# Kernel tuning notes

Hardware: AMD Instinct MI355X
Metric: run time of the kernel (lower is better)

The kernel has to match this reference:

```python
import jax, jax.numpy as jnp
import numpy as np
from jax import lax

B, D, H, W, C = 2, 144, 64, 160, 32
P = 300000
EPS = 1e-4   # scn BatchNormLeakyReLU default eps
LEAK = 0.2


def setup_inputs() -> dict:
    key = jax.random.key(0)
    ks = jax.random.split(key, 10)
    features = jax.random.normal(ks[0], (P, C), jnp.float32)
    b = jax.random.randint(ks[1], (P, 1), 0, B)
    x = jax.random.randint(ks[2], (P, 1), 0, D)
    y = jax.random.randint(ks[3], (P, 1), 0, H)
    z = jax.random.randint(ks[4], (P, 1), 0, W)
    coords = jnp.concatenate([b, x, y, z], axis=1).astype(jnp.int32)

    def conv_w(k, cin, cout):
        return jax.random.normal(k, (2, 2, 2, cin, cout), jnp.float32) / np.float32(np.sqrt(8 * cin))

    return {
        "features": features, "coords": coords,
        "w1": conv_w(ks[5], C, 64),  "g1": jnp.ones((64,), jnp.float32),  "b1": jnp.zeros((64,), jnp.float32),
        "w2": conv_w(ks[6], 64, 96), "g2": jnp.ones((96,), jnp.float32),  "b2": jnp.zeros((96,), jnp.float32),
        "w3": conv_w(ks[7], 96, 128),"g3": jnp.ones((128,), jnp.float32), "b3": jnp.zeros((128,), jnp.float32),
        "w4": conv_w(ks[8], 128, 1),
    }


def _densify(features, coords):
    # scn.InputLayer mode=4: average features of duplicate coordinates.
    lin = ((coords[:, 0] * D + coords[:, 1]) * H + coords[:, 2]) * W + coords[:, 3]
    grid = jnp.zeros((B * D * H * W, C), features.dtype).at[lin].add(features)
    cnt = jnp.zeros((B * D * H * W,), features.dtype).at[lin].add(1.0)
    grid = grid / jnp.maximum(cnt, 1.0)[:, None]
    x = grid.reshape(B, D, H, W, C)
    mask = (cnt > 0).astype(features.dtype).reshape(B, D, H, W, 1)
    return x, mask


def _conv2s2(x, w):
    # scn.Convolution(dim=3, filter=2, stride=2, bias=False): inactive inputs are zero,
    # so dense VALID conv reproduces values at active output sites exactly.
    return lax.conv_general_dilated(x, w, (2, 2, 2), 'VALID',
                                    dimension_numbers=('NDHWC', 'DHWIO', 'NDHWC'))


def _downsample_mask(mask):
    # Output site is active iff any input in its 2x2x2 window is active.
    return lax.reduce_window(mask, 0.0, lax.max, (1, 2, 2, 2, 1), (1, 2, 2, 2, 1), 'VALID')


def _block(x, mask, w, gamma, beta):
    x = _conv2s2(x, w)
    mask = _downsample_mask(mask)
    n = jnp.maximum(jnp.sum(mask), 1.0)
    # x is exactly zero at inactive sites, so sums over all sites == sums over active sites.
    mean = jnp.sum(x, axis=(0, 1, 2, 3)) / n
    var = jnp.sum(x * x, axis=(0, 1, 2, 3)) / n - mean * mean
    y = (x - mean) * (gamma * lax.rsqrt(var + EPS)) + beta
    y = jnp.where(y > 0, y, LEAK * y) * mask   # LeakyReLU on active sites, zero elsewhere
    return y, mask


def reference(features, coords, w1, g1, b1, w2, g2, b2, w3, g3, b3, w4):
    x, mask = _densify(features, coords)
    x, mask = _block(x, mask, w1, g1, b1)
    x, mask = _block(x, mask, w2, g2, b2)
    x, mask = _block(x, mask, w3, g3, b3)
    x = _conv2s2(x, w4)                 # [B, 9, 4, 10, 1]
    mask = _downsample_mask(mask)
    return jax.nn.sigmoid(x) * mask     # sigmoid of features; inactive sites zeroed
```

## Files before the change

kernel.cpp:

```cpp
#include <hip/hip_runtime.h>
#include <math.h>

#define PNUM 300000
#define B_ 2
#define D0 144
#define H0 64
#define W0 160
#define NVOX (B_*D0*H0*W0)

#define D1 72
#define H1 32
#define W1 80
#define N1S (B_*D1*H1*W1)

#define D2 36
#define H2 16
#define W2 40
#define N2S (B_*D2*H2*W2)

#define D3 18
#define H3 8
#define W3 20
#define N3S (B_*D3*H3*W3)

#define D4 9
#define H4 4
#define W4 10
#define N4S (B_*D4*H4*W4)

#define EPS_ 1e-4f
#define LEAK_ 0.2f

typedef __attribute__((ext_vector_type(8))) short v8s;
typedef __attribute__((ext_vector_type(4))) float v4f;

typedef unsigned short ushort_t;
typedef unsigned int uint_t;
typedef unsigned long long ull_t;

__device__ __forceinline__ ushort_t f2b(float f) {
  union { float f; uint_t u; } x; x.f = f;
  uint_t r = x.u + 0x7FFFu + ((x.u >> 16) & 1u);
  return (ushort_t)(r >> 16);
}
__device__ __forceinline__ float b2f(ushort_t h) {
  union { uint_t u; float f; } x; x.u = ((uint_t)h) << 16; return x.f;
}
__device__ __forceinline__ uint_t bn2(uint_t w, float s0, float h0, float s1, float h1,
                                      float msk) {
  float v0 = b2f((ushort_t)(w & 0xffff));
  float v1 = b2f((ushort_t)(w >> 16));
  v0 = fmaf(v0, s0, h0); v1 = fmaf(v1, s1, h1);
  v0 = fmaxf(v0, LEAK_ * v0) * msk;
  v1 = fmaxf(v1, LEAK_ * v1) * msk;
  return (uint_t)f2b(v0) | ((uint_t)f2b(v1) << 16);
}

template <int DD, int HH, int WW>
__device__ __forceinline__ int okey(int p) {
  int b = p / (DD*HH*WW); int r = p - b*(DD*HH*WW);
  int x = r / (HH*WW); r -= x*(HH*WW);
  int y = r / WW; int z = r - y*WW;
  return (((((b*(DD/2) + (x >> 1))*(HH/2) + (y >> 1))*(WW/2)) + (z >> 1)) << 3)
         | ((x & 1) << 2) | ((y & 1) << 1) | (z & 1);
}

#define OFF_CNT     0
#define OFF_STATS   2949120
#define OFF_CURSOR  2965504
#define OFF_DKLIST  5914624
#define OFF_WT1     6514624
#define OFF_WT2     6522816
#define OFF_WT3     6555584
#define OFF_AFEATB  6621120
#define OFF_X1B     11421120
#define OFF_X2B     23217600
#define OFF_X3B     26166720
#define OFF_M1      26535360
#define OFF_M2      26904000
#define OFF_M3      26950080

#define ST_S1P  0
#define ST_Q1P  2560
#define ST_S2P  5120
#define ST_Q2P  7424
#define ST_S3P  9728
#define ST_Q3P  12032
#define ST_N2P  14336
#define ST_N3P  14368
#define ST_GCUR 14400
#define ST_PK   14404

__device__ __forceinline__ int voxkey(int b, int x, int y, int z) {
  int p = ((b*D1 + (x >> 1))*H1 + (y >> 1))*W1 + (z >> 1);
  int oct = ((x & 1) << 2) | ((y & 1) << 1) | (z & 1);
  return p*8 + oct;
}

#define NB_COUNT 1172
#define NB_PREPW 832
#define NB_STZ   16
__global__ __launch_bounds__(256) void k_front(
    const int* __restrict__ coords, int* __restrict__ cnt,
    const float* __restrict__ w1, const float* __restrict__ w2,
    const float* __restrict__ w3,
    ushort_t* __restrict__ wt1, ushort_t* __restrict__ wt2,
    ushort_t* __restrict__ wt3, float* __restrict__ stz) {
  int bb = blockIdx.x, t = threadIdx.x;
  if (bb < NB_COUNT) {
    int i = bb * 256 + t;
    if (i < PNUM) {
      int4 c = *(const int4*)(coords + i*4);
      atomicAdd(&cnt[voxkey(c.x, c.y, c.z, c.w)], 1);
    }
  } else if (bb < NB_COUNT + NB_PREPW) {
    int idx = (bb - NB_COUNT) * 256 + t;
    if (idx < 16384) {
      int c = idx >> 11, r = idx & 2047;
      int co = r >> 5, kk = r & 31;
      wt1[idx] = f2b(w1[(c*32 + kk)*64 + co]);
    } else if (idx < 16384 + 65536) {
      int i = idx - 16384;
      int c = i >> 12, r = i & 4095;
      int co = r >> 5, kk = r & 31;
      int k = c*32 + kk;
      wt2[i] = (co < 96) ? f2b(w2[k*96 + co]) : 0;
    } else {
      int i = idx - 81920;
      int c = i >> 12, r = i & 4095;
      int co = r >> 5, kk = r & 31;
      int k = c*32 + kk;
      int ch = k >> 7, ci = k & 127;
      wt3[i] = (ci < 96) ? f2b(w3[(ch*96 + ci)*128 + co]) : 0;
    }
  } else {
    int off = ((bb - NB_COUNT - NB_PREPW) * 256 + t) * 4;
    *(float4*)(stz + off) = make_float4(0.f, 0.f, 0.f, 0.f);
  }
}

__global__ __launch_bounds__(1024) void k_alloc(const int* __restrict__ cnt,
                                                int* __restrict__ cursor,
                                                float* __restrict__ m1b,
                                                int* __restrict__ dklist,
                                                int* __restrict__ gcur,
                                                ull_t* __restrict__ pkctr) {
  __shared__ ull_t wsum[16];
  __shared__ int slotBase;
  __shared__ ull_t pkBase;
  int t = threadIdx.x;
  int idx0 = blockIdx.x * 16384 + t * 16;
  int c[16];
  int tsum = 0, dup = 0;
#pragma unroll
  for (int j = 0; j < 4; j++) {
    int4 cv = *(const int4*)(cnt + idx0 + j*4);
    c[j*4+0] = cv.x; c[j*4+1] = cv.y; c[j*4+2] = cv.z; c[j*4+3] = cv.w;
    tsum += cv.x + cv.y + cv.z + cv.w;
  }
#pragma unroll
  for (int j = 0; j < 16; j++) dup += (c[j] > 1) ? 1 : 0;
  uint_t m0 = 0, m1m = 0;
#pragma unroll
  for (int j = 0; j < 8; j++) { if (c[j] > 0) m0 |= (1u << j); }
#pragma unroll
  for (int j = 0; j < 8; j++) { if (c[8+j] > 0) m1m |= (1u << j); }
  int pa = ((m0 != 0) ? 1 : 0) + ((m1m != 0) ? 1 : 0);
  ull_t sv = ((ull_t)(uint_t)tsum << 32) | (ull_t)(uint_t)((pa << 16) | dup);
  int lane = t & 63, wid = t >> 6;
  ull_t incl = sv;
#pragma unroll
  for (int o = 1; o < 64; o <<= 1) {
    ull_t v = __shfl_up(incl, o);
    if (lane >= o) incl += v;
  }
  if (lane == 63) wsum[wid] = incl;
  __syncthreads();
  if (t == 0) {
    ull_t tot = 0;
#pragma unroll
    for (int w = 0; w < 16; w++) { ull_t v = wsum[w]; wsum[w] = tot; tot += v; }
    slotBase = atomicAdd(gcur, (int)(tot >> 32));
    uint_t pk = (uint_t)(tot & 0xffffffffULL);
    pkBase = atomicAdd(pkctr, ((ull_t)(pk >> 16) << 32) | (ull_t)(pk & 0xffff));
  }
  __syncthreads();
  ull_t excl = wsum[wid] + incl - sv;
  int st = slotBase + (int)(excl >> 32);
  uint_t pkl = (uint_t)(excl & 0xffffffffULL);
  int koff = (int)(pkBase & 0xffffffffULL) + (int)(pkl & 0xffff);
#pragma unroll
  for (int j = 0; j < 4; j++) {
    int4 sv2;
    sv2.x = st; st += c[j*4+0];
    sv2.y = st; st += c[j*4+1];
    sv2.z = st; st += c[j*4+2];
    sv2.w = st; st += c[j*4+3];
    *(int4*)(cursor + idx0 + j*4) = sv2;
  }
  int p0 = idx0 >> 3;
  m1b[okey<D1,H1,W1>(p0)]     = (m0 != 0) ? 1.f : 0.f;
  m1b[okey<D1,H1,W1>(p0 + 1)] = (m1m != 0) ? 1.f : 0.f;
#pragma unroll
  for (int j = 0; j < 16; j++)
    if (c[j] > 1) dklist[koff++] = idx0 + j;
}

__global__ __launch_bounds__(256) void k_scatter(const int* __restrict__ coords,
                                                 const float* __restrict__ feat,
                                                 const int* __restrict__ cnt,
                                                 int* __restrict__ cursor,
                                                 ushort_t* __restrict__ afb) {
  int i = blockIdx.x * 256 + threadIdx.x;
  if (i >= PNUM) return;
  int4 c = *(const int4*)(coords + i*4);
  int key = voxkey(c.x, c.y, c.z, c.w);
  int slot = atomicAdd(&cursor[key], 1);
  float inv = 1.f / (float)cnt[key];
  const float4* fp = (const float4*)(feat + (size_t)i * 32);
  uint_t o[16];
#pragma unroll
  for (int q = 0; q < 8; q++) {
    float4 v = fp[q];
    o[q*2]   = (uint_t)f2b(v.x*inv) | ((uint_t)f2b(v.y*inv) << 16);
    o[q*2+1] = (uint_t)f2b(v.z*inv) | ((uint_t)f2b(v.w*inv) << 16);
  }
  uint4* dst = (uint4*)(afb + (size_t)slot * 32);
  dst[0] = make_uint4(o[0], o[1], o[2], o[3]);
  dst[1] = make_uint4(o[4], o[5], o[6], o[7]);
  dst[2] = make_uint4(o[8], o[9], o[10], o[11]);
  dst[3] = make_uint4(o[12], o[13], o[14], o[15]);
}

__global__ __launch_bounds__(256) void k_davg(const int* __restrict__ cnt,
                                              const int* __restrict__ cursor,
                                              const int* __restrict__ dklist,
                                              const int* __restrict__ ndup,
                                              ushort_t* __restrict__ afb) {
  int gid = blockIdx.x * 256 + threadIdx.x;
  int j = gid >> 3;
  if (j >= ndup[0]) return;
  int key = dklist[j];
  int c = cnt[key];
  int s0 = cursor[key] - c;
  int q = (gid & 7) * 4;
  float a0 = 0.f, a1 = 0.f, a2 = 0.f, a3 = 0.f;
  for (int i = 0; i < c; i++) {
    uint2 u = *(const uint2*)(afb + (size_t)(s0 + i) * 32 + q);
    a0 += b2f((ushort_t)(u.x & 0xffff)); a1 += b2f((ushort_t)(u.x >> 16));
    a2 += b2f((ushort_t)(u.y & 0xffff)); a3 += b2f((ushort_t)(u.y >> 16));
  }
  uint2 o;
  o.x = (uint_t)f2b(a0) | ((uint_t)f2b(a1) << 16);
  o.y = (uint_t)f2b(a2) | ((uint_t)f2b(a3) << 16);
  *(uint2*)(afb + (size_t)s0 * 32 + q) = o;
}

__global__ __launch_bounds__(256) void k_conv1m(
    const ushort_t* __restrict__ afb, const int* __restrict__ cnt,
    const int* __restrict__ cursor, const ushort_t* __restrict__ wtg,
    ushort_t* __restrict__ x1b, float* __restrict__ sp, float* __restrict__ qp) {
  __shared__ __align__(16) ushort_t wlds[16384];
  __shared__ int cst[128*9];
  __shared__ int okl[128];
  __shared__ int pact[128];
  __shared__ float redS[4][64], redQ[4][64];
  int t = threadIdx.x;
#pragma unroll
  for (int i = 0; i < 8; i++)
    ((uint4*)wlds)[t + i*256] = ((const uint4*)wtg)[t + i*256];
  if (t < 128) {
    int p = blockIdx.x * 128 + t;
    okl[t] = okey<D1,H1,W1>(p);
    const int4* cp = (const int4*)(cnt + (size_t)p*8);
    const int4* up = (const int4*)(cursor + (size_t)p*8);
    int4 c0 = cp[0], c1 = cp[1], u0 = up[0], u1 = up[1];
    cst[t*9 + 0] = (c0.x > 0) ? (u0.x - c0.x) : -1;
    cst[t*9 + 1] = (c0.y > 0) ? (u0.y - c0.y) : -1;
    cst[t*9 + 2] = (c0.z > 0) ? (u0.z - c0.z) : -1;
    cst[t*9 + 3] = (c0.w > 0) ? (u0.w - c0.w) : -1;
    cst[t*9 + 4] = (c1.x > 0) ? (u1.x - c1.x) : -1;
    cst[t*9 + 5] = (c1.y > 0) ? (u1.y - c1.y) : -1;
    cst[t*9 + 6] = (c1.z > 0) ? (u1.z - c1.z) : -1;
    cst[t*9 + 7] = (c1.w > 0) ? (u1.w - c1.w) : -1;
    pact[t] = (c0.x + c0.y + c0.z + c0.w + c1.x + c1.y + c1.z + c1.w) > 0 ? 1 : 0;
  }
  __syncthreads();
  int lane = t & 63, wv = t >> 6;
  int l15 = lane & 15, q = lane >> 4;
  int SB = wv * 32;
  v8s a[8][2];
#pragma unroll
  for (int c = 0; c < 8; c++) {
#pragma unroll
    for (int mt = 0; mt < 2; mt++) {
      int site = SB + mt*16 + l15;
      int sp2 = cst[site*9 + c];
      v8s av = {0,0,0,0,0,0,0,0};
      if (sp2 >= 0) av = *(const v8s*)(afb + (size_t)sp2*32 + q*8);
      a[c][mt] = av;
    }
  }
  v4f acc[2][4];
#pragma unroll
  for (int i = 0; i < 2; i++)
#pragma unroll
    for (int j = 0; j < 4; j++) acc[i][j] = (v4f){0.f, 0.f, 0.f, 0.f};
#pragma unroll
  for (int c = 0; c < 8; c++) {
    v8s b[4];
#pragma unroll
    for (int nt = 0; nt < 4; nt++)
      b[nt] = *(const v8s*)&wlds[c*2048 + (nt*16 + l15)*32 + q*8];
#pragma unroll
    for (int mt = 0; mt < 2; mt++)
#pragma unroll
      for (int nt = 0; nt < 4; nt++)
        acc[mt][nt] = __builtin_amdgcn_mfma_f32_16x16x32_bf16(a[c][mt], b[nt], acc[mt][nt], 0, 0, 0);
  }
  float ss[4] = {0,0,0,0}, sq[4] = {0,0,0,0};
#pragma unroll
  for (int mt = 0; mt < 2; mt++) {
#pragma unroll
    for (int nt = 0; nt < 4; nt++) {
#pragma unroll
      for (int r = 0; r < 4; r++) {
        int sl = SB + mt*16 + q*4 + r;
        ushort_t h = f2b(acc[mt][nt][r]);
        float v = b2f(h);
        if (pact[sl]) x1b[(size_t)okl[sl]*64 + nt*16 + l15] = h;
        ss[nt] += v; sq[nt] += v*v;
      }
    }
  }
#pragma unroll
  for (int nt = 0; nt < 4; nt++) {
    float v1 = ss[nt], v2 = sq[nt];
    v1 += __shfl_xor(v1, 16); v1 += __shfl_xor(v1, 32);
    v2 += __shfl_xor(v2, 16); v2 += __shfl_xor(v2, 32);
    if (lane < 16) { redS[wv][nt*16 + l15] = v1; redQ[wv][nt*16 + l15] = v2; }
  }
  __syncthreads();
  if (t < 64) {
    float s = redS[0][t] + redS[1][t] + redS[2][t] + redS[3][t];
    float qq = redQ[0][t] + redQ[1][t] + redQ[2][t] + redQ[3][t];
    int row = (blockIdx.x & 31) * 80;
    atomicAdd(&sp[row + t], s);
    atomicAdd(&qp[row + t], qq);
  }
}

template <int CSTRIDE, int CIN_REAL, bool NINT, int NROW, int INSTR,
          int DO, int HO, int WO>
__global__ __launch_bounds__(256) void k_convm(
    const ushort_t* __restrict__ xin, const float* __restrict__ mprev,
    const ushort_t* __restrict__ wtg,
    const float* __restrict__ gam, const float* __restrict__ bet,
    const float* __restrict__ spin, const float* __restrict__ qpin,
    const void* __restrict__ ncnt, const float* __restrict__ npin,
    ushort_t* __restrict__ xout, float* __restrict__ osum, float* __restrict__ osq,
    float* __restrict__ mout, float* __restrict__ npart) {
  const int NCHUNK = CSTRIDE / 4;
  __shared__ __align__(16) float sc[CSTRIDE], sh[CSTRIDE];
  __shared__ float cmask[64*9];
  __shared__ int okl[64];
  __shared__ float redS[4][64], redQ[4][64];
  int t = threadIdx.x;
  if (t < CSTRIDE) {
    float scv = 0.f, shv = 0.f;
    if (t < CIN_REAL) {
      float n;
      if (NINT) n = fmaxf((float)((const int*)ncnt)[0], 1.0f);
      else {
        float nn = 0.f;
        for (int r = 0; r < 32; r++) nn += npin[r];
        n = fmaxf(nn, 1.0f);
      }
      float s1 = 0.f, q1 = 0.f;
      for (int r = 0; r < NROW; r++) { s1 += spin[r*INSTR + t]; q1 += qpin[r*INSTR + t]; }
      float mean = s1 / n;
      float var = q1 / n - mean * mean;
      float s = gam[t] * rsqrtf(var + EPS_);
      scv = s; shv = bet[t] - mean * s;
    }
    sc[t] = scv; sh[t] = shv;
  }
#pragma unroll
  for (int ii = 0; ii < 2; ii++) {
    int idx = t + ii*256;
    cmask[(idx >> 3)*9 + (idx & 7)] = mprev[(size_t)blockIdx.x * 512 + idx];
  }
  if (t < 64) okl[t] = okey<DO,HO,WO>(blockIdx.x * 64 + t);
  __syncthreads();
  int lane = t & 63, wv = t >> 6;
  int l15 = lane & 15, q = lane >> 4;
  int SB = (wv & 1) * 32, NB = (wv >> 1) * 64;
  size_t gbase = (size_t)blockIdx.x * 512;
  v4f acc[2][4];
#pragma unroll
  for (int i = 0; i < 2; i++)
#pragma unroll
    for (int j = 0; j < 4; j++) acc[i][j] = (v4f){0.f, 0.f, 0.f, 0.f};
  uint4 rawN[2]; float mskN[2]; v8s bN[4];
#pragma unroll
  for (int mt = 0; mt < 2; mt++) {
    int site = SB + mt*16 + l15;
    float m = cmask[site*9];
    uint4 rv = make_uint4(0, 0, 0, 0);
    if (m > 0.f) rv = *(const uint4*)(xin + (gbase + site*8) * CSTRIDE + q*8);
    rawN[mt] = rv; mskN[mt] = m;
  }
#pragma unroll
  for (int nt = 0; nt < 4; nt++)
    bN[nt] = *(const v8s*)(wtg + (NB + nt*16 + l15)*32 + q*8);
#pragma unroll
  for (int c = 0; c < NCHUNK; c++) {
    uint4 raw[2] = {rawN[0], rawN[1]};
    float mskc[2] = {mskN[0], mskN[1]};
    v8s b[4] = {bN[0], bN[1], bN[2], bN[3]};
    if (c + 1 < NCHUNK) {
      int ch1 = ((c+1) * 32) / CSTRIDE;
      int cio1 = ((c+1) * 32) % CSTRIDE + q * 8;
#pragma unroll
      for (int mt = 0; mt < 2; mt++) {
        int site = SB + mt*16 + l15;
        float m = cmask[site*9 + ch1];
        uint4 rv = make_uint4(0, 0, 0, 0);
        if (m > 0.f) rv = *(const uint4*)(xin + (gbase + site*8 + ch1) * CSTRIDE + cio1);
        rawN[mt] = rv; mskN[mt] = m;
      }
#pragma unroll
      for (int nt = 0; nt < 4; nt++)
        bN[nt] = *(const v8s*)(wtg + (size_t)(c+1)*4096 + (NB + nt*16 + l15)*32 + q*8);
    }
    int cio = (c * 32) % CSTRIDE + q * 8;
    float4 sc0 = *(const float4*)&sc[cio];
    float4 sc1 = *(const float4*)&sc[cio + 4];
    float4 sh0 = *(const float4*)&sh[cio];
    float4 sh1 = *(const float4*)&sh[cio + 4];
    v8s a[2];
#pragma unroll
    for (int mt = 0; mt < 2; mt++) {
      int4 pk;
      pk.x = (int)bn2(raw[mt].x, sc0.x, sh0.x, sc0.y, sh0.y, mskc[mt]);
      pk.y = (int)bn2(raw[mt].y, sc0.z, sh0.z, sc0.w, sh0.w, mskc[mt]);
      pk.z = (int)bn2(raw[mt].z, sc1.x, sh1.x, sc1.y, sh1.y, mskc[mt]);
      pk.w = (int)bn2(raw[mt].w, sc1.z, sh1.z, sc1.w, sh1.w, mskc[mt]);
      a[mt] = *(v8s*)&pk;
    }
#pragma unroll
    for (int mt = 0; mt < 2; mt++)
#pragma unroll
      for (int nt = 0; nt < 4; nt++)
        acc[mt][nt] = __builtin_amdgcn_mfma_f32_16x16x32_bf16(a[mt], b[nt], acc[mt][nt], 0, 0, 0);
  }
  float ss[4] = {0,0,0,0}, sq[4] = {0,0,0,0};
#pragma unroll
  for (int mt = 0; mt < 2; mt++) {
#pragma unroll
    for (int nt = 0; nt < 4; nt++) {
#pragma unroll
      for (int r = 0; r < 4; r++) {
        int sl = SB + mt*16 + q*4 + r;
        ushort_t h = f2b(acc[mt][nt][r]);
        float v = b2f(h);
        xout[(size_t)okl[sl]*128 + NB + nt*16 + l15] = h;
        ss[nt] += v; sq[nt] += v*v;
      }
    }
  }
  if (t < 64) {
    bool act = false;
#pragma unroll
    for (int ch = 0; ch < 8; ch++) act |= (cmask[t*9 + ch] > 0.f);
    mout[okl[t]] = act ? 1.f : 0.f;
    unsigned long long bal = __ballot(act);
    if (t == 0) atomicAdd(&npart[blockIdx.x & 31], (float)__popcll(bal));
  }
#pragma unroll
  for (int nt = 0; nt < 4; nt++) {
    float v1 = ss[nt], v2 = sq[nt];
    v1 += __shfl_xor(v1, 16); v1 += __shfl_xor(v1, 32);
    v2 += __shfl_xor(v2, 16); v2 += __shfl_xor(v2, 32);
    if (lane < 16) { redS[wv][nt*16 + l15] = v1; redQ[wv][nt*16 + l15] = v2; }
  }
  __syncthreads();
  if (t < 128) {
    float s, qq;
    if (t < 64) { s = redS[0][t] + redS[1][t]; qq = redQ[0][t] + redQ[1][t]; }
    else        { s = redS[2][t-64] + redS[3][t-64]; qq = redQ[2][t-64] + redQ[3][t-64]; }
    int row = (blockIdx.x & 15) * 144;
    atomicAdd(&osum[row + t], s);
    atomicAdd(&osq[row + t], qq);
  }
}

__global__ __launch_bounds__(256) void k_final(
    const ushort_t* __restrict__ x3b, const float* __restrict__ m3b,
    const float* __restrict__ w4, const float* __restrict__ gam,
    const float* __restrict__ bet, const float* __restrict__ spin,
    const float* __restrict__ qpin, const float* __restrict__ npin,
    float* __restrict__ out) {
  __shared__ float sc[128], sh[128];
  __shared__ float msk[8];
  __shared__ float red[256];
  int t = threadIdx.x;
  if (t < 128) {
    float nn = 0.f;
    for (int r = 0; r < 32; r++) nn += npin[r];
    float n = fmaxf(nn, 1.0f);
    float s1 = 0.f, q1 = 0.f;
    for (int r = 0; r < 16; r++) { s1 += spin[r*144 + t]; q1 += qpin[r*144 + t]; }
    float mean = s1 / n;
    float var = q1 / n - mean * mean;
    float s = gam[t] * rsqrtf(var + EPS_);
    sc[t] = s; sh[t] = bet[t] - mean * s;
  }
  int g = blockIdx.x;
  if (t < 8) msk[t] = m3b[g*8 + t];
  __syncthreads();
  float acc = 0.f;
#pragma unroll
  for (int ii = 0; ii < 4; ii++) {
    int k = t + ii*256;
    int ch = k >> 7, ci = k & 127;
    float v = b2f(x3b[(size_t)(g*8 + ch)*128 + ci]);
    v = v * sc[ci] + sh[ci];
    v = (v > 0.f ? v : LEAK_ * v) * msk[ch];
    acc += v * w4[k];
  }
  red[t] = acc;
  __syncthreads();
  if (t < 128) red[t] += red[t + 128];
  __syncthreads();
  if (t < 64) {
    float v = red[t] + red[t + 64];
#pragma unroll
    for (int off = 32; off > 0; off >>= 1) v += __shfl_down(v, off);
    if (t == 0) {
      float any = (msk[0] + msk[1] + msk[2] + msk[3] + msk[4] + msk[5] + msk[6] + msk[7]) > 0.f ? 1.f : 0.f;
      out[g] = any / (1.0f + expf(-v));
    }
  }
}

extern "C" void kernel_launch(void* const* d_in, const int* in_sizes, int n_in,
                              void* d_out, int out_size, void* d_ws, size_t ws_size,
                              hipStream_t stream) {
  (void)in_sizes; (void)n_in; (void)out_size; (void)ws_size;
  const float* feat = (const float*)d_in[0];
  const int*   crd  = (const int*)d_in[1];
  const float* w1 = (const float*)d_in[2];
  const float* g1 = (const float*)d_in[3];
  const float* b1 = (const float*)d_in[4];
  const float* w2 = (const float*)d_in[5];
  const float* g2 = (const float*)d_in[6];
  const float* b2 = (const float*)d_in[7];
  const float* w3 = (const float*)d_in[8];
  const float* g3 = (const float*)d_in[9];
  const float* b3 = (const float*)d_in[10];
  const float* w4 = (const float*)d_in[11];
  float* out = (float*)d_out;
  float* ws  = (float*)d_ws;

  int*      cnt    = (int*)(ws + OFF_CNT);
  float*    st     = ws + OFF_STATS;
  int*      cursor = (int*)(ws + OFF_CURSOR);
  int*      dklist = (int*)(ws + OFF_DKLIST);
  ushort_t* wt1g   = (ushort_t*)(ws + OFF_WT1);
  ushort_t* wt2g   = (ushort_t*)(ws + OFF_WT2);
  ushort_t* wt3g   = (ushort_t*)(ws + OFF_WT3);
  ushort_t* afb    = (ushort_t*)(ws + OFF_AFEATB);
  ushort_t* x1b    = (ushort_t*)(ws + OFF_X1B);
  ushort_t* x2b    = (ushort_t*)(ws + OFF_X2B);
  ushort_t* x3b    = (ushort_t*)(ws + OFF_X3B);
  float*    m1b    = ws + OFF_M1;
  float*    m2b    = ws + OFF_M2;
  float*    m3b    = ws + OFF_M3;
  ull_t*    pkctr  = (ull_t*)(st + ST_PK);
  int*      ndup   = (int*)(st + ST_PK);
  int*      nactp  = (int*)(st + ST_PK + 1);

  hipMemsetAsync(cnt, 0, (size_t)NVOX * sizeof(int), stream);

  k_front<<<NB_COUNT + NB_PREPW + NB_STZ, 256, 0, stream>>>(
      crd, cnt, w1, w2, w3, wt1g, wt2g, wt3g, st);
  k_alloc<<<NVOX / 16384, 1024, 0, stream>>>(cnt, cursor, m1b, dklist,
                                             (int*)(st + ST_GCUR), pkctr);
  k_scatter<<<(PNUM + 255) / 256, 256, 0, stream>>>(crd, feat, cnt, cursor, afb);
  k_davg<<<4688, 256, 0, stream>>>(cnt, cursor, dklist, ndup, afb);
  k_conv1m<<<N1S / 128, 256, 0, stream>>>(afb, cnt, cursor, wt1g, x1b,
                                          st + ST_S1P, st + ST_Q1P);
  k_convm<64, 64, true, 32, 80, D2,H2,W2><<<N2S / 64, 256, 0, stream>>>(
      x1b, m1b, wt2g, g1, b1, st + ST_S1P, st + ST_Q1P, (const void*)nactp, nullptr,
      x2b, st + ST_S2P, st + ST_Q2P, m2b, st + ST_N2P);
  k_convm<128, 96, false, 16, 144, D3,H3,W3><<<N3S / 64, 256, 0, stream>>>(
      x2b, m2b, wt3g, g2, b2, st + ST_S2P, st + ST_Q2P, nullptr, st + ST_N2P,
      x3b, st + ST_S3P, st + ST_Q3P, m3b, st + ST_N3P);
  k_final<<<N4S, 256, 0, stream>>>(x3b, m3b, w4, g3, b3,
                                   st + ST_S3P, st + ST_Q3P, st + ST_N3P, out);
}
```

Measured before the change: 244.2 us.

## Fuse duplicate-voxel averaging into conv1 gather and drop davg kernel

Removes the k_davg kernel and the duplicate-key list built in k_alloc. Duplicate-coordinate sums are now accumulated directly while conv1 gathers its input, using per-site counts kept in shared memory. The scan in k_alloc is simplified to 32-bit with a separate active-count reduction. conv1 also iterates blocks in output-key order so x1b stores are contiguous, and it reuses the weight LDS for the reduction scratch. The cost is divergent extra loads inside the conv1 gather for duplicate sites, plus an added barrier.

```diff
diff --git a/kernel.cpp b/kernel.cpp
--- a/kernel.cpp
+++ b/kernel.cpp
@@ -68,7 +68,6 @@
 #define OFF_CNT     0
 #define OFF_STATS   2949120
 #define OFF_CURSOR  2965504
-#define OFF_DKLIST  5914624
 #define OFF_WT1     6514624
 #define OFF_WT2     6522816
 #define OFF_WT3     6555584
@@ -142,53 +141,49 @@
 __global__ __launch_bounds__(1024) void k_alloc(const int* __restrict__ cnt,
                                                 int* __restrict__ cursor,
                                                 float* __restrict__ m1b,
-                                                int* __restrict__ dklist,
                                                 int* __restrict__ gcur,
-                                                ull_t* __restrict__ pkctr) {
-  __shared__ ull_t wsum[16];
-  __shared__ int slotBase;
-  __shared__ ull_t pkBase;
+                                                int* __restrict__ nactp) {
+  __shared__ int wsum[16];
+  __shared__ int wpa[16];
+  __shared__ int blockBase;
   int t = threadIdx.x;
   int idx0 = blockIdx.x * 16384 + t * 16;
   int c[16];
-  int tsum = 0, dup = 0;
+  int tsum = 0;
 #pragma unroll
   for (int j = 0; j < 4; j++) {
     int4 cv = *(const int4*)(cnt + idx0 + j*4);
     c[j*4+0] = cv.x; c[j*4+1] = cv.y; c[j*4+2] = cv.z; c[j*4+3] = cv.w;
     tsum += cv.x + cv.y + cv.z + cv.w;
   }
-#pragma unroll
-  for (int j = 0; j < 16; j++) dup += (c[j] > 1) ? 1 : 0;
   uint_t m0 = 0, m1m = 0;
 #pragma unroll
   for (int j = 0; j < 8; j++) { if (c[j] > 0) m0 |= (1u << j); }
 #pragma unroll
   for (int j = 0; j < 8; j++) { if (c[8+j] > 0) m1m |= (1u << j); }
   int pa = ((m0 != 0) ? 1 : 0) + ((m1m != 0) ? 1 : 0);
-  ull_t sv = ((ull_t)(uint_t)tsum << 32) | (ull_t)(uint_t)((pa << 16) | dup);
   int lane = t & 63, wid = t >> 6;
-  ull_t incl = sv;
+  int incl = tsum;
 #pragma unroll
   for (int o = 1; o < 64; o <<= 1) {
-    ull_t v = __shfl_up(incl, o);
+    int v = __shfl_up(incl, o);
     if (lane >= o) incl += v;
   }
+  int pw = pa;
+#pragma unroll
+  for (int o = 1; o < 64; o <<= 1) pw += __shfl_xor(pw, o);
   if (lane == 63) wsum[wid] = incl;
+  if (lane == 0) wpa[wid] = pw;
   __syncthreads();
   if (t == 0) {
-    ull_t tot = 0;
-#pragma unroll
-    for (int w = 0; w < 16; w++) { ull_t v = wsum[w]; wsum[w] = tot; tot += v; }
-    slotBase = atomicAdd(gcur, (int)(tot >> 32));
-    uint_t pk = (uint_t)(tot & 0xffffffffULL);
-    pkBase = atomicAdd(pkctr, ((ull_t)(pk >> 16) << 32) | (ull_t)(pk & 0xffff));
-  }
-  __syncthreads();
-  ull_t excl = wsum[wid] + incl - sv;
-  int st = slotBase + (int)(excl >> 32);
-  uint_t pkl = (uint_t)(excl & 0xffffffffULL);
-  int koff = (int)(pkBase & 0xffffffffULL) + (int)(pkl & 0xffff);
+    int tot = 0, ptot = 0;
+#pragma unroll
+    for (int w = 0; w < 16; w++) { int v = wsum[w]; wsum[w] = tot; tot += v; ptot += wpa[w]; }
+    blockBase = atomicAdd(gcur, tot);
+    atomicAdd(nactp, ptot);
+  }
+  __syncthreads();
+  int st = blockBase + wsum[wid] + incl - tsum;
 #pragma unroll
   for (int j = 0; j < 4; j++) {
     int4 sv2;
@@ -201,9 +196,6 @@
   int p0 = idx0 >> 3;
   m1b[okey<D1,H1,W1>(p0)]     = (m0 != 0) ? 1.f : 0.f;
   m1b[okey<D1,H1,W1>(p0 + 1)] = (m1m != 0) ? 1.f : 0.f;
-#pragma unroll
-  for (int j = 0; j < 16; j++)
-    if (c[j] > 1) dklist[koff++] = idx0 + j;
 }
 
 __global__ __launch_bounds__(256) void k_scatter(const int* __restrict__ coords,
@@ -232,57 +224,39 @@
   dst[3] = make_uint4(o[12], o[13], o[14], o[15]);
 }
 
-__global__ __launch_bounds__(256) void k_davg(const int* __restrict__ cnt,
-                                              const int* __restrict__ cursor,
-                                              const int* __restrict__ dklist,
-                                              const int* __restrict__ ndup,
-                                              ushort_t* __restrict__ afb) {
-  int gid = blockIdx.x * 256 + threadIdx.x;
-  int j = gid >> 3;
-  if (j >= ndup[0]) return;
-  int key = dklist[j];
-  int c = cnt[key];
-  int s0 = cursor[key] - c;
-  int q = (gid & 7) * 4;
-  float a0 = 0.f, a1 = 0.f, a2 = 0.f, a3 = 0.f;
-  for (int i = 0; i < c; i++) {
-    uint2 u = *(const uint2*)(afb + (size_t)(s0 + i) * 32 + q);
-    a0 += b2f((ushort_t)(u.x & 0xffff)); a1 += b2f((ushort_t)(u.x >> 16));
-    a2 += b2f((ushort_t)(u.y & 0xffff)); a3 += b2f((ushort_t)(u.y >> 16));
-  }
-  uint2 o;
-  o.x = (uint_t)f2b(a0) | ((uint_t)f2b(a1) << 16);
-  o.y = (uint_t)f2b(a2) | ((uint_t)f2b(a3) << 16);
-  *(uint2*)(afb + (size_t)s0 * 32 + q) = o;
-}
-
 __global__ __launch_bounds__(256) void k_conv1m(
     const ushort_t* __restrict__ afb, const int* __restrict__ cnt,
     const int* __restrict__ cursor, const ushort_t* __restrict__ wtg,
     ushort_t* __restrict__ x1b, float* __restrict__ sp, float* __restrict__ qp) {
   __shared__ __align__(16) ushort_t wlds[16384];
   __shared__ int cst[128*9];
-  __shared__ int okl[128];
+  __shared__ ushort_t ccn[128*9];
   __shared__ int pact[128];
-  __shared__ float redS[4][64], redQ[4][64];
   int t = threadIdx.x;
 #pragma unroll
   for (int i = 0; i < 8; i++)
     ((uint4*)wlds)[t + i*256] = ((const uint4*)wtg)[t + i*256];
   if (t < 128) {
-    int p = blockIdx.x * 128 + t;
-    okl[t] = okey<D1,H1,W1>(p);
+    int ok = blockIdx.x * 128 + t;
+    int oct = ok & 7, qp2 = ok >> 3;
+    int b = qp2 / (D2*H2*W2); int r = qp2 - b*(D2*H2*W2);
+    int x2 = r / (H2*W2); r -= x2*(H2*W2);
+    int y2 = r / W2; int z2 = r - y2*W2;
+    int x = 2*x2 + ((oct >> 2) & 1);
+    int y = 2*y2 + ((oct >> 1) & 1);
+    int z = 2*z2 + (oct & 1);
+    int p = ((b*D1 + x)*H1 + y)*W1 + z;
     const int4* cp = (const int4*)(cnt + (size_t)p*8);
     const int4* up = (const int4*)(cursor + (size_t)p*8);
     int4 c0 = cp[0], c1 = cp[1], u0 = up[0], u1 = up[1];
-    cst[t*9 + 0] = (c0.x > 0) ? (u0.x - c0.x) : -1;
-    cst[t*9 + 1] = (c0.y > 0) ? (u0.y - c0.y) : -1;
-    cst[t*9 + 2] = (c0.z > 0) ? (u0.z - c0.z) : -1;
-    cst[t*9 + 3] = (c0.w > 0) ? (u0.w - c0.w) : -1;
-    cst[t*9 + 4] = (c1.x > 0) ? (u1.x - c1.x) : -1;
-    cst[t*9 + 5] = (c1.y > 0) ? (u1.y - c1.y) : -1;
-    cst[t*9 + 6] = (c1.z > 0) ? (u1.z - c1.z) : -1;
-    cst[t*9 + 7] = (c1.w > 0) ? (u1.w - c1.w) : -1;
+    cst[t*9 + 0] = (c0.x > 0) ? (u0.x - c0.x) : -1; ccn[t*9 + 0] = (ushort_t)c0.x;
+    cst[t*9 + 1] = (c0.y > 0) ? (u0.y - c0.y) : -1; ccn[t*9 + 1] = (ushort_t)c0.y;
+    cst[t*9 + 2] = (c0.z > 0) ? (u0.z - c0.z) : -1; ccn[t*9 + 2] = (ushort_t)c0.z;
+    cst[t*9 + 3] = (c0.w > 0) ? (u0.w - c0.w) : -1; ccn[t*9 + 3] = (ushort_t)c0.w;
+    cst[t*9 + 4] = (c1.x > 0) ? (u1.x - c1.x) : -1; ccn[t*9 + 4] = (ushort_t)c1.x;
+    cst[t*9 + 5] = (c1.y > 0) ? (u1.y - c1.y) : -1; ccn[t*9 + 5] = (ushort_t)c1.y;
+    cst[t*9 + 6] = (c1.z > 0) ? (u1.z - c1.z) : -1; ccn[t*9 + 6] = (ushort_t)c1.z;
+    cst[t*9 + 7] = (c1.w > 0) ? (u1.w - c1.w) : -1; ccn[t*9 + 7] = (ushort_t)c1.w;
     pact[t] = (c0.x + c0.y + c0.z + c0.w + c1.x + c1.y + c1.z + c1.w) > 0 ? 1 : 0;
   }
   __syncthreads();
@@ -295,10 +269,30 @@
 #pragma unroll
     for (int mt = 0; mt < 2; mt++) {
       int site = SB + mt*16 + l15;
-      int sp2 = cst[site*9 + c];
-      v8s av = {0,0,0,0,0,0,0,0};
-      if (sp2 >= 0) av = *(const v8s*)(afb + (size_t)sp2*32 + q*8);
-      a[c][mt] = av;
+      int info = cst[site*9 + c];
+      int cn = ccn[site*9 + c];
+      uint4 u = make_uint4(0, 0, 0, 0);
+      if (info >= 0) {
+        u = *(const uint4*)(afb + (size_t)info*32 + q*8);
+        if (cn > 1) {
+          float f0 = b2f((ushort_t)(u.x & 0xffff)), f1 = b2f((ushort_t)(u.x >> 16));
+          float f2 = b2f((ushort_t)(u.y & 0xffff)), f3 = b2f((ushort_t)(u.y >> 16));
+          float f4 = b2f((ushort_t)(u.z & 0xffff)), f5 = b2f((ushort_t)(u.z >> 16));
+          float f6 = b2f((ushort_t)(u.w & 0xffff)), f7 = b2f((ushort_t)(u.w >> 16));
+          for (int i = 1; i < cn; i++) {
+            uint4 w = *(const uint4*)(afb + (size_t)(info + i)*32 + q*8);
+            f0 += b2f((ushort_t)(w.x & 0xffff)); f1 += b2f((ushort_t)(w.x >> 16));
+            f2 += b2f((ushort_t)(w.y & 0xffff)); f3 += b2f((ushort_t)(w.y >> 16));
+            f4 += b2f((ushort_t)(w.z & 0xffff)); f5 += b2f((ushort_t)(w.z >> 16));
+            f6 += b2f((ushort_t)(w.w & 0xffff)); f7 += b2f((ushort_t)(w.w >> 16));
+          }
+          u.x = (uint_t)f2b(f0) | ((uint_t)f2b(f1) << 16);
+          u.y = (uint_t)f2b(f2) | ((uint_t)f2b(f3) << 16);
+          u.z = (uint_t)f2b(f4) | ((uint_t)f2b(f5) << 16);
+          u.w = (uint_t)f2b(f6) | ((uint_t)f2b(f7) << 16);
+        }
+      }
+      a[c][mt] = *(v8s*)&u;
     }
   }
   v4f acc[2][4];
@@ -318,6 +312,7 @@
       for (int nt = 0; nt < 4; nt++)
         acc[mt][nt] = __builtin_amdgcn_mfma_f32_16x16x32_bf16(a[c][mt], b[nt], acc[mt][nt], 0, 0, 0);
   }
+  size_t okbase = (size_t)blockIdx.x * 128;
   float ss[4] = {0,0,0,0}, sq[4] = {0,0,0,0};
 #pragma unroll
   for (int mt = 0; mt < 2; mt++) {
@@ -328,22 +323,25 @@
         int sl = SB + mt*16 + q*4 + r;
         ushort_t h = f2b(acc[mt][nt][r]);
         float v = b2f(h);
-        if (pact[sl]) x1b[(size_t)okl[sl]*64 + nt*16 + l15] = h;
+        if (pact[sl]) x1b[(okbase + sl)*64 + nt*16 + l15] = h;
         ss[nt] += v; sq[nt] += v*v;
       }
     }
   }
+  __syncthreads();
+  float* redS = (float*)wlds;
+  float* redQ = redS + 256;
 #pragma unroll
   for (int nt = 0; nt < 4; nt++) {
     float v1 = ss[nt], v2 = sq[nt];
     v1 += __shfl_xor(v1, 16); v1 += __shfl_xor(v1, 32);
     v2 += __shfl_xor(v2, 16); v2 += __shfl_xor(v2, 32);
-    if (lane < 16) { redS[wv][nt*16 + l15] = v1; redQ[wv][nt*16 + l15] = v2; }
+    if (lane < 16) { redS[wv*64 + nt*16 + l15] = v1; redQ[wv*64 + nt*16 + l15] = v2; }
   }
   __syncthreads();
   if (t < 64) {
-    float s = redS[0][t] + redS[1][t] + redS[2][t] + redS[3][t];
-    float qq = redQ[0][t] + redQ[1][t] + redQ[2][t] + redQ[3][t];
+    float s = redS[t] + redS[64 + t] + redS[128 + t] + redS[192 + t];
+    float qq = redQ[t] + redQ[64 + t] + redQ[128 + t] + redQ[192 + t];
     int row = (blockIdx.x & 31) * 80;
     atomicAdd(&sp[row + t], s);
     atomicAdd(&qp[row + t], qq);
@@ -566,7 +564,6 @@
   int*      cnt    = (int*)(ws + OFF_CNT);
   float*    st     = ws + OFF_STATS;
   int*      cursor = (int*)(ws + OFF_CURSOR);
-  int*      dklist = (int*)(ws + OFF_DKLIST);
   ushort_t* wt1g   = (ushort_t*)(ws + OFF_WT1);
   ushort_t* wt2g   = (ushort_t*)(ws + OFF_WT2);
   ushort_t* wt3g   = (ushort_t*)(ws + OFF_WT3);
@@ -577,18 +574,15 @@
   float*    m1b    = ws + OFF_M1;
   float*    m2b    = ws + OFF_M2;
   float*    m3b    = ws + OFF_M3;
-  ull_t*    pkctr  = (ull_t*)(st + ST_PK);
-  int*      ndup   = (int*)(st + ST_PK);
-  int*      nactp  = (int*)(st + ST_PK + 1);
+  int*      nactp  = (int*)(st + ST_PK);
 
   hipMemsetAsync(cnt, 0, (size_t)NVOX * sizeof(int), stream);
 
   k_front<<<NB_COUNT + NB_PREPW + NB_STZ, 256, 0, stream>>>(
       crd, cnt, w1, w2, w3, wt1g, wt2g, wt3g, st);
-  k_alloc<<<NVOX / 16384, 1024, 0, stream>>>(cnt, cursor, m1b, dklist,
-                                             (int*)(st + ST_GCUR), pkctr);
+  k_alloc<<<NVOX / 16384, 1024, 0, stream>>>(cnt, cursor, m1b,
+                                             (int*)(st + ST_GCUR), nactp);
   k_scatter<<<(PNUM + 255) / 256, 256, 0, stream>>>(crd, feat, cnt, cursor, afb);
-  k_davg<<<4688, 256, 0, stream>>>(cnt, cursor, dklist, ndup, afb);
   k_conv1m<<<N1S / 128, 256, 0, stream>>>(afb, cnt, cursor, wt1g, x1b,
                                           st + ST_S1P, st + ST_Q1P);
   k_convm<64, 64, true, 32, 80, D2,H2,W2><<<N2S / 64, 256, 0, stream>>>(
```

Measured after the change: 241.8 us. Within noise of the previous version (-1.0%).
